# Performance work log

Hardware: AMD Instinct MI355X
Metric: run time of the kernel (lower is better)

## Reference

```python
import jax, jax.numpy as jnp
import numpy as np

N_NODES = 100000
N_EDGES = 3200000
D_FEAT = 512
D_HID = 64
D_LAT = 16
N_CLASS = 10
N_FLOW = 10
K_PROP = 10
ALPHA_TELEPORT = 0.1


def setup_inputs() -> dict:
    key = jax.random.key(0)
    ks = jax.random.split(key, 8)
    x = jax.random.normal(ks[0], (N_NODES, D_FEAT), jnp.float32)
    edge_index = jax.random.randint(ks[1], (2, N_EDGES), 0, N_NODES)
    p_c = jax.random.uniform(ks[2], (N_CLASS,), jnp.float32) + 0.1
    p_c = p_c / p_c.sum()
    W1 = jax.random.normal(ks[3], (D_FEAT, D_HID), jnp.float32) / np.sqrt(D_FEAT).astype(np.float32)
    b1 = jnp.zeros((D_HID,), jnp.float32)
    W2 = jax.random.normal(ks[4], (D_HID, D_LAT), jnp.float32) / np.sqrt(D_HID).astype(np.float32)
    b2 = jnp.zeros((D_LAT,), jnp.float32)
    flow_z0 = jax.random.normal(ks[5], (N_FLOW, N_CLASS, D_LAT), jnp.float32) * 0.1
    flow_alpha_prime = jax.random.normal(ks[6], (N_FLOW, N_CLASS, 1), jnp.float32) * 0.1
    flow_beta = jax.random.normal(ks[7], (N_FLOW, N_CLASS, 1), jnp.float32) * 0.1
    return dict(x=x, edge_index=edge_index, p_c=p_c, W1=W1, b1=b1, W2=W2, b2=b2,
                flow_z0=flow_z0, flow_alpha_prime=flow_alpha_prime, flow_beta=flow_beta)


def _batched_radial_log_prob(z, flow_z0, flow_alpha_prime, flow_beta):
    # Per-class batched radial flow (invertible pyro-style parameterization).
    # z: [N, D] -> log_q: [N, C]
    C, D = flow_z0.shape[1], flow_z0.shape[2]
    zz = jnp.broadcast_to(z[None], (C, z.shape[0], D))  # [C, N, D]
    sum_logdet = jnp.zeros((C, z.shape[0]), z.dtype)
    for l in range(flow_z0.shape[0]):  # small fixed number of flow layers
        z0 = flow_z0[l][:, None, :]                               # [C,1,D]
        alpha = jax.nn.softplus(flow_alpha_prime[l])[:, None, :]  # [C,1,1]
        beta_hat = -alpha + jax.nn.softplus(flow_beta[l])[:, None, :]
        dz = zz - z0
        r = jnp.sqrt(jnp.sum(dz * dz, axis=-1, keepdims=True))    # [C,N,1]
        h = 1.0 / (alpha + r)
        bh = beta_hat * h
        zz = zz + bh * dz
        logdet = (D - 1) * jnp.log1p(bh) + jnp.log1p(bh - beta_hat * r * h * h)
        sum_logdet = sum_logdet + logdet[..., 0]
    log_base = -0.5 * jnp.sum(zz * zz, axis=-1) - 0.5 * D * jnp.log(2.0 * jnp.pi)
    return (log_base + sum_logdet).T  # [N, C]


def _appnp(beta_ft, edge_index, n_nodes):
    # APPNP with self loops and symmetric gcn normalization over edge list.
    src = jnp.concatenate([edge_index[0], jnp.arange(n_nodes)])
    dst = jnp.concatenate([edge_index[1], jnp.arange(n_nodes)])
    deg = jax.ops.segment_sum(jnp.ones_like(src, dtype=beta_ft.dtype), dst, num_segments=n_nodes)
    dinv = jnp.where(deg > 0, jax.lax.rsqrt(jnp.maximum(deg, 1.0)), 0.0)
    norm = (dinv[src] * dinv[dst])[:, None]  # [E+N, 1]
    x0 = beta_ft
    b = beta_ft
    for _ in range(K_PROP):
        agg = jax.ops.segment_sum(norm * b[src], dst, num_segments=n_nodes)
        b = (1.0 - ALPHA_TELEPORT) * agg + ALPHA_TELEPORT * x0
    return b


def reference(x, edge_index, p_c, W1, b1, W2, b2, flow_z0, flow_alpha_prime, flow_beta):
    h = jax.nn.relu(x @ W1 + b1)           # input_encoder (dropout inactive at eval)
    z = h @ W2 + b2                        # latent_encoder, [N, D_LAT]
    log_q = _batched_radial_log_prob(z, flow_z0, flow_alpha_prime, flow_beta)
    log_q_per_class = log_q + jnp.log(p_c)[None, :]
    log_scale = 0.5 * D_LAT * jnp.log(4.0 * jnp.pi)  # 'latent-new' evidence scale
    beta_ft = jnp.exp(jnp.clip(log_q_per_class + log_scale, -30.0, 30.0))
    beta = _appnp(beta_ft, edge_index, x.shape[0])
    alpha = 1.0 + beta
    soft = alpha / jnp.sum(alpha, axis=-1, keepdims=True)
    hard = jnp.argmax(soft, axis=-1)
    return hard[:, None], soft
```

## Files before the change

kernel.cpp:

```cpp
#include <hip/hip_runtime.h>
#include <math.h>
#include <limits.h>

#define DF 512
#define DH 64
#define DL 16
#define NC 10
#define NF 10
#define KPROP 10

#define BSH 7
#define BW  (1 << BSH)
#define MAXB 1024
#define TILE 16384

__device__ __forceinline__ float softplus_(float x){
  return fmaxf(x, 0.0f) + log1pf(expf(-fabsf(x)));
}

#define BM 64
#define BN 64
#define BK 32
__global__ __launch_bounds__(256) void k_gemm1z(const float* __restrict__ x,
    const float* __restrict__ W1, const float* __restrict__ b1,
    const float* __restrict__ W2, const float* __restrict__ b2,
    float* __restrict__ z, int N)
{
  __shared__ float smem[2*BK*(BM+4)];
  float (*At)[BM+4] = (float(*)[BM+4])smem;
  float (*Bs)[BN+4] = (float(*)[BN+4])(smem + BK*(BM+4));
  __shared__ float W2s[DH][DL];
  __shared__ float b2s[DL];
  const int tid = threadIdx.x;
  for (int i = tid; i < DH*DL; i += 256) W2s[i>>4][i&15] = W2[i];
  if (tid < DL) b2s[tid] = b2[tid];
  const int tx = tid & 15, ty = tid >> 4;
  const int row0 = blockIdx.x * BM;
  float acc[4][4] = {};
  for (int k0 = 0; k0 < DF; k0 += BK) {
    #pragma unroll
    for (int i = 0; i < 2; ++i) {
      int idx = tid + i*256;
      int r  = idx >> 3;
      int kk = (idx & 7) << 2;
      int row = row0 + r;
      float4 va = make_float4(0.f,0.f,0.f,0.f);
      if (row < N) va = *(const float4*)&x[(size_t)row*DF + k0 + kk];
      At[kk+0][r]=va.x; At[kk+1][r]=va.y; At[kk+2][r]=va.z; At[kk+3][r]=va.w;
      int r2 = idx >> 4;
      int c4 = (idx & 15) << 2;
      float4 vb = *(const float4*)&W1[(size_t)(k0+r2)*DH + c4];
      Bs[r2][c4+0]=vb.x; Bs[r2][c4+1]=vb.y; Bs[r2][c4+2]=vb.z; Bs[r2][c4+3]=vb.w;
    }
    __syncthreads();
    #pragma unroll
    for (int kk = 0; kk < BK; ++kk) {
      float4 av = *(const float4*)&At[kk][ty<<2];
      float4 bv = *(const float4*)&Bs[kk][tx<<2];
      float a4[4]={av.x,av.y,av.z,av.w};
      float b4[4]={bv.x,bv.y,bv.z,bv.w};
      #pragma unroll
      for (int i=0;i<4;++i)
        #pragma unroll
        for (int j=0;j<4;++j) acc[i][j] = fmaf(a4[i], b4[j], acc[i][j]);
    }
    __syncthreads();
  }
  float4 bias = ((const float4*)b1)[tx];
  float bias4[4] = {bias.x, bias.y, bias.z, bias.w};
  float (*hs)[BM+4] = (float(*)[BM+4])smem;
  #pragma unroll
  for (int i=0;i<4;++i){
    #pragma unroll
    for (int j=0;j<4;++j)
      hs[(ty<<2)+i][(tx<<2)+j] = fmaxf(acc[i][j] + bias4[j], 0.0f);
  }
  __syncthreads();
  int row = tid >> 2, lg = tid & 3;
  float4 zacc = ((const float4*)b2s)[lg];
  #pragma unroll 8
  for (int k = 0; k < DH; ++k){
    float hv = hs[row][k];
    float4 wv = *(const float4*)&W2s[k][lg<<2];
    zacc.x = fmaf(hv, wv.x, zacc.x);
    zacc.y = fmaf(hv, wv.y, zacc.y);
    zacc.z = fmaf(hv, wv.z, zacc.z);
    zacc.w = fmaf(hv, wv.w, zacc.w);
  }
  int grow = row0 + row;
  if (grow < N) ((float4*)z)[(size_t)grow*4 + lg] = zacc;
}

__global__ __launch_bounds__(256) void k_flow2(const float* __restrict__ z,
    const float* __restrict__ pc, const float* __restrict__ z0g,
    const float* __restrict__ apg, const float* __restrict__ fbg,
    const float* __restrict__ dinv,
    float* __restrict__ x0, float* __restrict__ c0, float* __restrict__ y0, int N)
{
  __shared__ float z0s[NF][NC][DL];
  __shared__ float alps[NF][NC];
  __shared__ float bhs[NF][NC];
  __shared__ float lpc[NC];
  int tid = threadIdx.x;
  for (int i = tid; i < NF*NC*DL; i += 256)
    z0s[(i>>4)/NC][(i>>4)%NC][i&15] = z0g[i];
  if (tid < NF*NC){
    int l = tid/NC, c = tid%NC;
    float al = softplus_(apg[tid]);
    alps[l][c] = al;
    bhs[l][c]  = -al + softplus_(fbg[tid]);
  }
  if (tid < NC) lpc[tid] = __logf(pc[tid]);
  __syncthreads();

  int idx = blockIdx.x*256 + tid;
  int n = idx >> 4, c = idx & 15;
  if (n >= N) return;
  float dn = dinv[n];
  if (c >= NC){ x0[idx] = 0.f; c0[idx] = 0.f; y0[idx] = 0.f; return; }

  float zz[DL];
  const float4* z4 = (const float4*)z;
  #pragma unroll
  for (int q=0; q<4; ++q){
    float4 v = z4[(size_t)n*4 + q];
    zz[q*4+0]=v.x; zz[q*4+1]=v.y; zz[q*4+2]=v.z; zz[q*4+3]=v.w;
  }
  const float NEGHALFD_LOG2PI = -14.703016531274762f;
  const float LOGSCALE        =  20.248193975754326f;
  float sld = 0.f;
  #pragma unroll 1
  for (int l=0; l<NF; ++l){
    float al = alps[l][c], bhat = bhs[l][c];
    float dz[DL]; float r2 = 0.f;
    #pragma unroll
    for (int d=0; d<DL; ++d){ float t = zz[d] - z0s[l][c][d]; dz[d]=t; r2 = fmaf(t,t,r2); }
    float r  = sqrtf(r2);
    float hh = 1.0f/(al + r);
    float bh = bhat*hh;
    #pragma unroll
    for (int d=0; d<DL; ++d) zz[d] = fmaf(bh, dz[d], zz[d]);
    sld += 15.0f*__logf(1.0f + bh) + __logf(1.0f + bh - bhat*r*hh*hh);
  }
  float q2 = 0.f;
  #pragma unroll
  for (int d=0; d<DL; ++d) q2 = fmaf(zz[d], zz[d], q2);
  float v = -0.5f*q2 + NEGHALFD_LOG2PI + sld + lpc[c] + LOGSCALE;
  v = fminf(fmaxf(v, -30.f), 30.f);
  float xv = __expf(v);
  x0[idx] = xv;
  c0[idx] = dn*xv;
  y0[idx] = 0.1f*dn*xv;
}

__global__ __launch_bounds__(256) void k_bhist(const int* __restrict__ dst,
    int* __restrict__ bCnt, int E, int B)
{
  __shared__ int hh[MAXB];
  int tid = threadIdx.x;
  for (int b = tid; b < B; b += 256) hh[b] = 0;
  __syncthreads();
  for (int i = blockIdx.x*256 + tid; i < E; i += gridDim.x*256)
    atomicAdd(&hh[dst[i] >> BSH], 1);
  __syncthreads();
  for (int b = tid; b < B; b += 256) if (hh[b]) atomicAdd(&bCnt[b], hh[b]);
}

__global__ void k_bscan(const int* __restrict__ bCnt, int* __restrict__ bOff, int B){
  if (blockIdx.x==0 && threadIdx.x==0){
    int run = 0;
    for (int b=0;b<B;++b){ bOff[b]=run; run+=bCnt[b]; }
    bOff[B]=run;
  }
}

__global__ __launch_bounds__(256) void k_bscatter(const int* __restrict__ src,
    const int* __restrict__ dst, const int* __restrict__ bOff,
    int* __restrict__ bCur, int* __restrict__ bp, int E, int B)
{
  __shared__ int hc[MAXB];
  __shared__ int hb[MAXB];
  int tid = threadIdx.x;
  int base = blockIdx.x * TILE;
  int lim  = base + TILE; if (lim > E) lim = E;
  for (int b = tid; b < B; b += 256) hc[b] = 0;
  __syncthreads();
  for (int i = base + tid; i < lim; i += 256)
    atomicAdd(&hc[dst[i] >> BSH], 1);
  __syncthreads();
  for (int b = tid; b < B; b += 256){
    int c = hc[b];
    hb[b] = c ? atomicAdd(&bCur[b], c) : 0;
    hc[b] = 0;
  }
  __syncthreads();
  for (int i = base + tid; i < lim; i += 256){
    int d = dst[i];
    int b = d >> BSH;
    int pos = bOff[b] + hb[b] + atomicAdd(&hc[b], 1);
    bp[pos] = (src[i] << BSH) | (d & (BW-1));
  }
}

__global__ __launch_bounds__(256) void k_bdeg(const int* __restrict__ bp,
    const int* __restrict__ bOff, int* __restrict__ deg,
    float* __restrict__ dinv, float* __restrict__ dinv2, int N)
{
  __shared__ int cur[BW];
  int tid = threadIdx.x;
  int b = blockIdx.x;
  if (tid < BW) cur[tid] = 0;
  __syncthreads();
  int s = bOff[b], e = bOff[b+1];
  for (int i = s + tid; i < e; i += 256)
    atomicAdd(&cur[bp[i] & (BW-1)], 1);
  __syncthreads();
  int node = (b << BSH) + tid;
  if (tid < BW && node < N){
    int d = cur[tid] + 1;
    deg[node] = d;
    float dv = 1.0f / sqrtf((float)d);
    dinv[node]  = dv;
    dinv2[node] = dv*dv;
  }
}

__global__ __launch_bounds__(256) void k_scan_part(const int* __restrict__ deg,
    int* __restrict__ part, int N){
  __shared__ int sd[256];
  int base = blockIdx.x*1024;
  int tid = threadIdx.x;
  int s = 0;
  #pragma unroll
  for (int i=0;i<4;++i){ int idx = base + tid*4 + i; if (idx < N) s += deg[idx]; }
  sd[tid] = s; __syncthreads();
  for (int ofs=128; ofs>0; ofs>>=1){ if (tid<ofs) sd[tid]+=sd[tid+ofs]; __syncthreads(); }
  if (tid==0) part[blockIdx.x] = sd[0];
}

__global__ void k_scan_top(int* part, int nb){
  if (blockIdx.x==0 && threadIdx.x==0){
    int run = 0;
    for (int i=0;i<nb;++i){ int v = part[i]; part[i] = run; run += v; }
  }
}

__global__ __launch_bounds__(256) void k_scan_final(const int* __restrict__ deg,
    const int* __restrict__ part, int* __restrict__ off, int N, int E)
{
  __shared__ int sc[256];
  int base = blockIdx.x*1024;
  int tid = threadIdx.x;
  int v[4]; int s = 0;
  #pragma unroll
  for (int i=0;i<4;++i){ int idx = base + tid*4 + i; v[i] = (idx<N)?deg[idx]:0; s += v[i]; }
  sc[tid] = s; __syncthreads();
  for (int ofs=1; ofs<256; ofs<<=1){
    int t = (tid>=ofs) ? sc[tid-ofs] : 0;
    __syncthreads();
    sc[tid] += t;
    __syncthreads();
  }
  int ex = sc[tid] - s + part[blockIdx.x];
  #pragma unroll
  for (int i=0;i<4;++i){
    int idx = base + tid*4 + i;
    if (idx < N){
      off[idx] = ex;
      if (idx == N-1) off[N] = ex + v[i];
      ex += v[i];
    }
  }
}

__global__ __launch_bounds__(256) void k_place(const int* __restrict__ bp,
    const int* __restrict__ bOff, const int* __restrict__ off,
    int* __restrict__ csr, int N)
{
  __shared__ int cur[BW];
  int tid = threadIdx.x;
  int b = blockIdx.x;
  int node0 = b << BSH;
  if (tid < BW){
    cur[tid] = 1;
    int node = node0 + tid;
    if (node < N) csr[off[node]] = node;
  }
  __syncthreads();
  int s = bOff[b], e = bOff[b+1];
  for (int i = s + tid; i < e; i += 256){
    int v  = bp[i];
    int dl = v & (BW-1);
    int sn = v >> BSH;
    int d  = node0 + dl;
    int p  = off[d] + atomicAdd(&cur[dl], 1);
    csr[p] = sn;
  }
}

__global__ __launch_bounds__(256) void k_rank(int* __restrict__ csr,
    const int* __restrict__ off, int N)
{
  int wid  = (blockIdx.x*256 + threadIdx.x) >> 6;
  int lane = threadIdx.x & 63;
  if (wid >= N) return;
  int s = off[wid], e = off[wid+1];
  int d = e - s;
  if (d <= 1) return;
  if (d <= 64){
    int v = (lane < d) ? csr[s+lane] : INT_MAX;
    int rank = 0;
    for (int j = 0; j < d; ++j){
      int bv = __shfl(v, j);
      rank += (bv < v) || (bv == v && j < lane);
    }
    if (lane < d) csr[s+rank] = v;
  } else if (d <= 256){
    int v0 = (lane      < d) ? csr[s+lane      ] : INT_MAX;
    int v1 = (lane+64   < d) ? csr[s+lane+64   ] : INT_MAX;
    int v2 = (lane+128  < d) ? csr[s+lane+128  ] : INT_MAX;
    int v3 = (lane+192  < d) ? csr[s+lane+192  ] : INT_MAX;
    int r0=0,r1=0,r2=0,r3=0;
    for (int j = 0; j < d; ++j){
      int slot = j >> 6, jl = j & 63;
      int bv = (slot==0) ? __shfl(v0,jl) : (slot==1) ? __shfl(v1,jl)
             : (slot==2) ? __shfl(v2,jl) : __shfl(v3,jl);
      r0 += (bv < v0) || (bv == v0 && j < lane);
      r1 += (bv < v1) || (bv == v1 && j < lane+64);
      r2 += (bv < v2) || (bv == v2 && j < lane+128);
      r3 += (bv < v3) || (bv == v3 && j < lane+192);
    }
    if (lane      < d) csr[s+r0]=v0;
    if (lane+64   < d) csr[s+r1]=v1;
    if (lane+128  < d) csr[s+r2]=v2;
    if (lane+192  < d) csr[s+r3]=v3;
  } else {
    if (lane == 0){
      for (int i = s+1; i < e; ++i){
        int key = csr[i]; int j = i-1;
        while (j >= s && csr[j] > key){ csr[j+1] = csr[j]; --j; }
        csr[j+1] = key;
      }
    }
  }
}

__global__ __launch_bounds__(256) void k_prop(const float* __restrict__ cin,
    const float* __restrict__ y0, const float* __restrict__ dinv2,
    float* __restrict__ cout,
    const int* __restrict__ csr, const int* __restrict__ off, int N)
{
  int t = blockIdx.x*256 + threadIdx.x;
  int n = t >> 4, sub = t & 15, q = sub & 3, part = sub >> 2;
  if (n >= N) return;
  const float4* c4 = (const float4*)cin;
  int s = off[n], e = off[n+1], d = e - s;
  int lo = s + ((d*part) >> 2);
  int hi = s + ((d*(part+1)) >> 2);
  float4 a0 = make_float4(0.f,0.f,0.f,0.f);
  float4 a1 = make_float4(0.f,0.f,0.f,0.f);
  int i = lo;
  for (; i+4 <= hi; i += 4){
    int s0=csr[i], s1=csr[i+1], s2=csr[i+2], s3=csr[i+3];
    float4 v0 = c4[(size_t)s0*4 + q];
    float4 v1 = c4[(size_t)s1*4 + q];
    float4 v2 = c4[(size_t)s2*4 + q];
    float4 v3 = c4[(size_t)s3*4 + q];
    a0.x+=v0.x; a0.y+=v0.y; a0.z+=v0.z; a0.w+=v0.w;
    a1.x+=v1.x; a1.y+=v1.y; a1.z+=v1.z; a1.w+=v1.w;
    a0.x+=v2.x; a0.y+=v2.y; a0.z+=v2.z; a0.w+=v2.w;
    a1.x+=v3.x; a1.y+=v3.y; a1.z+=v3.z; a1.w+=v3.w;
  }
  for (; i < hi; ++i){
    float4 v = c4[(size_t)csr[i]*4 + q];
    a0.x+=v.x; a0.y+=v.y; a0.z+=v.z; a0.w+=v.w;
  }
  float ax = a0.x+a1.x, ay = a0.y+a1.y, az = a0.z+a1.z, aw = a0.w+a1.w;
  ax += __shfl_xor(ax, 4, 16);  ay += __shfl_xor(ay, 4, 16);
  az += __shfl_xor(az, 4, 16);  aw += __shfl_xor(aw, 4, 16);
  ax += __shfl_xor(ax, 8, 16);  ay += __shfl_xor(ay, 8, 16);
  az += __shfl_xor(az, 8, 16);  aw += __shfl_xor(aw, 8, 16);
  if (part == 0){
    float w9 = 0.9f * dinv2[n];
    float4 yv = ((const float4*)y0)[(size_t)n*4 + q];
    float4 o;
    o.x = fmaf(w9, ax, yv.x);
    o.y = fmaf(w9, ay, yv.y);
    o.z = fmaf(w9, az, yv.z);
    o.w = fmaf(w9, aw, yv.w);
    ((float4*)cout)[(size_t)n*4 + q] = o;
  }
}

__global__ __launch_bounds__(256) void k_prop_final(const float* __restrict__ cin,
    const float* __restrict__ x0, const float* __restrict__ dinv,
    const int* __restrict__ csr, const int* __restrict__ off,
    float* __restrict__ out, int N)
{
  int t = blockIdx.x*256 + threadIdx.x;
  int n = t >> 4, sub = t & 15, q = sub & 3, part = sub >> 2;
  if (n >= N) return;
  const float4* c4 = (const float4*)cin;
  int s = off[n], e = off[n+1], d = e - s;
  int lo = s + ((d*part) >> 2);
  int hi = s + ((d*(part+1)) >> 2);
  float4 a0 = make_float4(0.f,0.f,0.f,0.f);
  float4 a1 = make_float4(0.f,0.f,0.f,0.f);
  int i = lo;
  for (; i+4 <= hi; i += 4){
    int s0=csr[i], s1=csr[i+1], s2=csr[i+2], s3=csr[i+3];
    float4 v0 = c4[(size_t)s0*4 + q];
    float4 v1 = c4[(size_t)s1*4 + q];
    float4 v2 = c4[(size_t)s2*4 + q];
    float4 v3 = c4[(size_t)s3*4 + q];
    a0.x+=v0.x; a0.y+=v0.y; a0.z+=v0.z; a0.w+=v0.w;
    a1.x+=v1.x; a1.y+=v1.y; a1.z+=v1.z; a1.w+=v1.w;
    a0.x+=v2.x; a0.y+=v2.y; a0.z+=v2.z; a0.w+=v2.w;
    a1.x+=v3.x; a1.y+=v3.y; a1.z+=v3.z; a1.w+=v3.w;
  }
  for (; i < hi; ++i){
    float4 v = c4[(size_t)csr[i]*4 + q];
    a0.x+=v.x; a0.y+=v.y; a0.z+=v.z; a0.w+=v.w;
  }
  float ax = a0.x+a1.x, ay = a0.y+a1.y, az = a0.z+a1.z, aw = a0.w+a1.w;
  ax += __shfl_xor(ax, 4, 16);  ay += __shfl_xor(ay, 4, 16);
  az += __shfl_xor(az, 4, 16);  aw += __shfl_xor(aw, 4, 16);
  ax += __shfl_xor(ax, 8, 16);  ay += __shfl_xor(ay, 8, 16);
  az += __shfl_xor(az, 8, 16);  aw += __shfl_xor(aw, 8, 16);
  if (part != 0) return;

  float w9 = 0.9f * dinv[n];
  float4 xv = ((const float4*)x0)[(size_t)n*4 + q];
  float4 al;
  al.x = fmaf(w9, ax, fmaf(0.1f, xv.x, 1.f));
  al.y = fmaf(w9, ay, fmaf(0.1f, xv.y, 1.f));
  al.z = fmaf(w9, az, fmaf(0.1f, xv.z, 1.f));
  al.w = fmaf(w9, aw, fmaf(0.1f, xv.w, 1.f));

  float sv = 0.f;
  if (q < 2)       sv = al.x + al.y + al.z + al.w;
  else if (q == 2) sv = al.x + al.y;
  sv += __shfl_xor(sv, 1, 4);
  sv += __shfl_xor(sv, 2, 4);

  float bv = -1e30f; int bi = 999;
  int cb = q*4;
  int nvalid = (q < 2) ? 4 : (q == 2 ? 2 : 0);
  float av[4] = {al.x, al.y, al.z, al.w};
  for (int j = 0; j < nvalid; ++j){
    if (av[j] > bv){ bv = av[j]; bi = cb + j; }
  }
  #pragma unroll
  for (int o = 1; o <= 2; o <<= 1){
    float vo = __shfl_xor(bv, o, 4);
    int  io  = __shfl_xor(bi, o, 4);
    if (vo > bv || (vo == bv && io < bi)){ bv = vo; bi = io; }
  }

  float inv = 1.0f / sv;
  size_t sb = (size_t)N + (size_t)n*NC;
  for (int j = 0; j < nvalid; ++j) out[sb + cb + j] = av[j] * inv;
  if (q == 0) out[n] = (float)bi;
}

extern "C" void kernel_launch(void* const* d_in, const int* in_sizes, int n_in,
                              void* d_out, int out_size, void* d_ws, size_t ws_size,
                              hipStream_t stream)
{
  const float* x  = (const float*)d_in[0];
  const int*   ei = (const int*)  d_in[1];
  const float* pc = (const float*)d_in[2];
  const float* W1 = (const float*)d_in[3];
  const float* b1 = (const float*)d_in[4];
  const float* W2 = (const float*)d_in[5];
  const float* b2 = (const float*)d_in[6];
  const float* z0 = (const float*)d_in[7];
  const float* ap = (const float*)d_in[8];
  const float* fb = (const float*)d_in[9];
  float* out = (float*)d_out;

  const int N = in_sizes[0] / DF;
  const int E = in_sizes[1] / 2;
  const int* src = ei;
  const int* dst = ei + E;
  const int B = (N + BW - 1) >> BSH;

  char* ws = (char*)d_ws;
  size_t o = 0;
  size_t region0 = (size_t)E*sizeof(int);
  if ((size_t)N*DL*sizeof(float) > region0) region0 = (size_t)N*DL*sizeof(float);
  int*   bp   = (int*)  (ws + o);
  float* z    = (float*)(ws + o);
  o += region0;
  int*   csr  = (int*)  (ws + o); o += (size_t)(E+N)*sizeof(int);
  float* x0   = (float*)(ws + o); o += (size_t)N*DL*sizeof(float);
  float* c0   = (float*)(ws + o); o += (size_t)N*DL*sizeof(float);
  float* y0   = (float*)(ws + o); o += (size_t)N*DL*sizeof(float);
  float* cA   = (float*)(ws + o); o += (size_t)N*DL*sizeof(float);
  float* cB   = (float*)(ws + o); o += (size_t)N*DL*sizeof(float);
  int*   deg  = (int*)  (ws + o); o += (size_t)N*sizeof(int);
  float* dinv = (float*)(ws + o); o += (size_t)N*sizeof(float);
  float* dinv2= (float*)(ws + o); o += (size_t)N*sizeof(float);
  int*   offs = (int*)  (ws + o); o += (size_t)(N+2)*sizeof(int);
  int*   part = (int*)  (ws + o); o += 4096;
  int*   bCnt = (int*)  (ws + o); o += MAXB*sizeof(int);
  int*   bOff = (int*)  (ws + o); o += (MAXB+1)*sizeof(int);
  int*   bCur = (int*)  (ws + o); o += MAXB*sizeof(int);

  const int TB = 256;
  int nb  = (N + 1023) / 1024;

  hipMemsetAsync(bCnt, 0, MAXB*sizeof(int), stream);
  hipMemsetAsync(bCur, 0, MAXB*sizeof(int), stream);
  k_bhist<<<512, TB, 0, stream>>>(dst, bCnt, E, B);
  k_bscan<<<1, 1, 0, stream>>>(bCnt, bOff, B);
  k_bscatter<<<(E + TILE - 1)/TILE, TB, 0, stream>>>(src, dst, bOff, bCur, bp, E, B);
  k_bdeg<<<B, TB, 0, stream>>>(bp, bOff, deg, dinv, dinv2, N);
  k_scan_part<<<nb, TB, 0, stream>>>(deg, part, N);
  k_scan_top<<<1, 1, 0, stream>>>(part, nb);
  k_scan_final<<<nb, TB, 0, stream>>>(deg, part, offs, N, E);
  k_place<<<B, TB, 0, stream>>>(bp, bOff, offs, csr, N);
  k_rank<<<(N + 3) / 4, TB, 0, stream>>>(csr, offs, N);

  k_gemm1z<<<(N + BM - 1) / BM, TB, 0, stream>>>(x, W1, b1, W2, b2, z, N);
  k_flow2<<<((N*DL) + TB - 1) / TB, TB, 0, stream>>>(z, pc, z0, ap, fb, dinv,
                                                     x0, c0, y0, N);

  int gP = ((N*16) + TB - 1) / TB;
  const float* cin = c0;
  for (int it = 0; it < KPROP-1; ++it){
    float* cout = (it & 1) ? cB : cA;
    k_prop<<<gP, TB, 0, stream>>>(cin, y0, dinv2, cout, csr, offs, N);
    cin = cout;
  }
  k_prop_final<<<gP, TB, 0, stream>>>(cin, x0, dinv, csr, offs, out, N);
}
```

Before: 772.8 us.

## Skip padded feature quarter in propagation and parallelize the small scans

```diff
diff --git a/kernel.cpp b/kernel.cpp
--- a/kernel.cpp
+++ b/kernel.cpp
@@ -166,12 +166,37 @@
   for (int b = tid; b < B; b += 256) if (hh[b]) atomicAdd(&bCnt[b], hh[b]);
 }
 
-__global__ void k_bscan(const int* __restrict__ bCnt, int* __restrict__ bOff, int B){
-  if (blockIdx.x==0 && threadIdx.x==0){
-    int run = 0;
-    for (int b=0;b<B;++b){ bOff[b]=run; run+=bCnt[b]; }
-    bOff[B]=run;
-  }
+__global__ __launch_bounds__(256) void k_scan_small(const int* __restrict__ in,
+    int* __restrict__ out, int n, int writeTotal)
+{
+  __shared__ int sd[1024];
+  int tid = threadIdx.x;
+  int orig[4];
+  #pragma unroll
+  for (int j = 0; j < 4; ++j){
+    int i = tid + j*256;
+    orig[j] = (i < n) ? in[i] : 0;
+    sd[i] = orig[j];
+  }
+  __syncthreads();
+  for (int ofs = 1; ofs < 1024; ofs <<= 1){
+    int vals[4];
+    #pragma unroll
+    for (int j = 0; j < 4; ++j){
+      int i = tid + j*256;
+      vals[j] = (i >= ofs) ? sd[i-ofs] : 0;
+    }
+    __syncthreads();
+    #pragma unroll
+    for (int j = 0; j < 4; ++j) sd[tid + j*256] += vals[j];
+    __syncthreads();
+  }
+  #pragma unroll
+  for (int j = 0; j < 4; ++j){
+    int i = tid + j*256;
+    if (i < n) out[i] = sd[i] - orig[j];
+  }
+  if (writeTotal && tid == 0) out[n] = sd[n-1];
 }
 
 __global__ __launch_bounds__(256) void k_bscatter(const int* __restrict__ src,
@@ -236,13 +261,6 @@
   sd[tid] = s; __syncthreads();
   for (int ofs=128; ofs>0; ofs>>=1){ if (tid<ofs) sd[tid]+=sd[tid+ofs]; __syncthreads(); }
   if (tid==0) part[blockIdx.x] = sd[0];
-}
-
-__global__ void k_scan_top(int* part, int nb){
-  if (blockIdx.x==0 && threadIdx.x==0){
-    int run = 0;
-    for (int i=0;i<nb;++i){ int v = part[i]; part[i] = run; run += v; }
-  }
 }
 
 __global__ __launch_bounds__(256) void k_scan_final(const int* __restrict__ deg,
@@ -351,7 +369,8 @@
     const int* __restrict__ csr, const int* __restrict__ off, int N)
 {
   int t = blockIdx.x*256 + threadIdx.x;
-  int n = t >> 4, sub = t & 15, q = sub & 3, part = sub >> 2;
+  int n = t / 12, sub = t - n*12;
+  int q = sub >> 2, part = sub & 3;
   if (n >= N) return;
   const float4* c4 = (const float4*)cin;
   int s = off[n], e = off[n+1], d = e - s;
@@ -376,10 +395,10 @@
     a0.x+=v.x; a0.y+=v.y; a0.z+=v.z; a0.w+=v.w;
   }
   float ax = a0.x+a1.x, ay = a0.y+a1.y, az = a0.z+a1.z, aw = a0.w+a1.w;
-  ax += __shfl_xor(ax, 4, 16);  ay += __shfl_xor(ay, 4, 16);
-  az += __shfl_xor(az, 4, 16);  aw += __shfl_xor(aw, 4, 16);
-  ax += __shfl_xor(ax, 8, 16);  ay += __shfl_xor(ay, 8, 16);
-  az += __shfl_xor(az, 8, 16);  aw += __shfl_xor(aw, 8, 16);
+  ax += __shfl_xor(ax, 1, 4);  ay += __shfl_xor(ay, 1, 4);
+  az += __shfl_xor(az, 1, 4);  aw += __shfl_xor(aw, 1, 4);
+  ax += __shfl_xor(ax, 2, 4);  ay += __shfl_xor(ay, 2, 4);
+  az += __shfl_xor(az, 2, 4);  aw += __shfl_xor(aw, 2, 4);
   if (part == 0){
     float w9 = 0.9f * dinv2[n];
     float4 yv = ((const float4*)y0)[(size_t)n*4 + q];
@@ -406,21 +425,23 @@
   int hi = s + ((d*(part+1)) >> 2);
   float4 a0 = make_float4(0.f,0.f,0.f,0.f);
   float4 a1 = make_float4(0.f,0.f,0.f,0.f);
-  int i = lo;
-  for (; i+4 <= hi; i += 4){
-    int s0=csr[i], s1=csr[i+1], s2=csr[i+2], s3=csr[i+3];
-    float4 v0 = c4[(size_t)s0*4 + q];
-    float4 v1 = c4[(size_t)s1*4 + q];
-    float4 v2 = c4[(size_t)s2*4 + q];
-    float4 v3 = c4[(size_t)s3*4 + q];
-    a0.x+=v0.x; a0.y+=v0.y; a0.z+=v0.z; a0.w+=v0.w;
-    a1.x+=v1.x; a1.y+=v1.y; a1.z+=v1.z; a1.w+=v1.w;
-    a0.x+=v2.x; a0.y+=v2.y; a0.z+=v2.z; a0.w+=v2.w;
-    a1.x+=v3.x; a1.y+=v3.y; a1.z+=v3.z; a1.w+=v3.w;
-  }
-  for (; i < hi; ++i){
-    float4 v = c4[(size_t)csr[i]*4 + q];
-    a0.x+=v.x; a0.y+=v.y; a0.z+=v.z; a0.w+=v.w;
+  if (q < 3){
+    int i = lo;
+    for (; i+4 <= hi; i += 4){
+      int s0=csr[i], s1=csr[i+1], s2=csr[i+2], s3=csr[i+3];
+      float4 v0 = c4[(size_t)s0*4 + q];
+      float4 v1 = c4[(size_t)s1*4 + q];
+      float4 v2 = c4[(size_t)s2*4 + q];
+      float4 v3 = c4[(size_t)s3*4 + q];
+      a0.x+=v0.x; a0.y+=v0.y; a0.z+=v0.z; a0.w+=v0.w;
+      a1.x+=v1.x; a1.y+=v1.y; a1.z+=v1.z; a1.w+=v1.w;
+      a0.x+=v2.x; a0.y+=v2.y; a0.z+=v2.z; a0.w+=v2.w;
+      a1.x+=v3.x; a1.y+=v3.y; a1.z+=v3.z; a1.w+=v3.w;
+    }
+    for (; i < hi; ++i){
+      float4 v = c4[(size_t)csr[i]*4 + q];
+      a0.x+=v.x; a0.y+=v.y; a0.z+=v.z; a0.w+=v.w;
+    }
   }
   float ax = a0.x+a1.x, ay = a0.y+a1.y, az = a0.z+a1.z, aw = a0.w+a1.w;
   ax += __shfl_xor(ax, 4, 16);  ay += __shfl_xor(ay, 4, 16);
@@ -513,11 +534,11 @@
   hipMemsetAsync(bCnt, 0, MAXB*sizeof(int), stream);
   hipMemsetAsync(bCur, 0, MAXB*sizeof(int), stream);
   k_bhist<<<512, TB, 0, stream>>>(dst, bCnt, E, B);
-  k_bscan<<<1, 1, 0, stream>>>(bCnt, bOff, B);
+  k_scan_small<<<1, TB, 0, stream>>>(bCnt, bOff, B, 1);
   k_bscatter<<<(E + TILE - 1)/TILE, TB, 0, stream>>>(src, dst, bOff, bCur, bp, E, B);
   k_bdeg<<<B, TB, 0, stream>>>(bp, bOff, deg, dinv, dinv2, N);
   k_scan_part<<<nb, TB, 0, stream>>>(deg, part, N);
-  k_scan_top<<<1, 1, 0, stream>>>(part, nb);
+  k_scan_small<<<1, TB, 0, stream>>>(part, part, nb, 0);
   k_scan_final<<<nb, TB, 0, stream>>>(deg, part, offs, N, E);
   k_place<<<B, TB, 0, stream>>>(bp, bOff, offs, csr, N);
   k_rank<<<(N + 3) / 4, TB, 0, stream>>>(csr, offs, N);
@@ -526,12 +547,13 @@
   k_flow2<<<((N*DL) + TB - 1) / TB, TB, 0, stream>>>(z, pc, z0, ap, fb, dinv,
                                                      x0, c0, y0, N);
 
-  int gP = ((N*16) + TB - 1) / TB;
+  int gP = ((N*12) + TB - 1) / TB;
   const float* cin = c0;
   for (int it = 0; it < KPROP-1; ++it){
     float* cout = (it & 1) ? cB : cA;
     k_prop<<<gP, TB, 0, stream>>>(cin, y0, dinv2, cout, csr, offs, N);
     cin = cout;
   }
-  k_prop_final<<<gP, TB, 0, stream>>>(cin, x0, dinv, csr, offs, out, N);
-}
+  int gF = ((N*16) + TB - 1) / TB;
+  k_prop_final<<<gF, TB, 0, stream>>>(cin, x0, dinv, csr, offs, out, N);
+}
```

Measured after the change: 741.8 us. 1.04x faster.
